# Optimization experiments

Hardware: AMD Instinct MI355X
Metric: run time of the kernel (lower is better)

## Reference

```python
import jax, jax.numpy as jnp
import numpy as np

D_MODEL = 1024
H = 16
D_H = D_MODEL // H


def setup_inputs() -> dict:
    key = jax.random.key(0)
    ks = jax.random.split(key, 10)
    B, T_dec, T_enc = 2, 2048, 2048
    s = 1.0 / np.sqrt(D_MODEL)
    return {
        "tgt": jax.random.normal(ks[0], (B, T_dec, D_MODEL), jnp.float32),
        "memory": jax.random.normal(ks[1], (B, T_enc, D_MODEL), jnp.float32),
        "W_q": jax.random.normal(ks[2], (D_MODEL, D_MODEL), jnp.float32) * s,
        "b_q": jnp.zeros((D_MODEL,), jnp.float32),
        "W_k": jax.random.normal(ks[3], (D_MODEL, D_MODEL), jnp.float32) * s,
        "b_k": jnp.zeros((D_MODEL,), jnp.float32),
        "W_v": jax.random.normal(ks[4], (D_MODEL, D_MODEL), jnp.float32) * s,
        "b_v": jnp.zeros((D_MODEL,), jnp.float32),
        "W_o": jax.random.normal(ks[5], (D_MODEL, D_MODEL), jnp.float32) * s,
        "b_o": jnp.zeros((D_MODEL,), jnp.float32),
    }


def reference(tgt, memory, W_q, b_q, W_k, b_k, W_v, b_v, W_o, b_o):
    B, T_dec, _ = tgt.shape
    T_enc = memory.shape[1]
    # Projections (nn.Linear: x @ W^T + b; here W stored as (in,out) so x @ W + b)
    Q = tgt @ W_q + b_q          # (B, T_dec, d_model)
    K = memory @ W_k + b_k       # (B, T_enc, d_model)
    V = memory @ W_v + b_v       # (B, T_enc, d_model)
    # split heads: (B, h, T, d_h)
    Q = Q.reshape(B, T_dec, H, D_H).transpose(0, 2, 1, 3)
    K = K.reshape(B, T_enc, H, D_H).transpose(0, 2, 1, 3)
    V = V.reshape(B, T_enc, H, D_H).transpose(0, 2, 1, 3)
    # scores (B, h, T_dec, T_enc)
    S = jnp.einsum("bhqd,bhkd->bhqk", Q, K) / jnp.sqrt(jnp.float32(D_H)).astype(Q.dtype)
    A = jax.nn.softmax(S, axis=-1)
    Y = jnp.einsum("bhqk,bhkd->bhqd", A, V)
    Y = Y.transpose(0, 2, 1, 3).reshape(B, T_dec, D_MODEL)
    return Y @ W_o + b_o
```

## Files before the change

kernel.cpp:

```cpp
#include <hip/hip_runtime.h>
#include <hip/hip_bf16.h>
#include <stdint.h>

typedef unsigned short u16;
typedef __attribute__((ext_vector_type(8))) short bf16x8;
typedef __attribute__((ext_vector_type(4))) short bf16x4;
typedef __attribute__((ext_vector_type(4))) float f32x4;

__device__ __forceinline__ float bf2f(u16 u) {
    union { unsigned int i; float f; } v; v.i = ((unsigned int)u) << 16; return v.f;
}
__device__ __forceinline__ u16 f2bf(float f) {
    union { float f; unsigned int i; } v; v.f = f;
    unsigned int x = v.i;
    return (u16)((x + 0x7fffu + ((x >> 16) & 1u)) >> 16);
}
__device__ __forceinline__ unsigned fbits(float f) {
    union { float f; unsigned int i; } v; v.f = f; return v.i;
}
__device__ __forceinline__ void async16(const void* g, void* lds) {
    __builtin_amdgcn_global_load_lds((const __attribute__((address_space(1))) void*)g,
                                     (__attribute__((address_space(3))) void*)lds,
                                     16, 0, 0);
}

#define QSCALE 0.18033688f

__global__ __launch_bounds__(256) void prep(
    const float* __restrict__ tgt, const float* __restrict__ mem,
    const float* __restrict__ Wq, const float* __restrict__ Wk,
    const float* __restrict__ Wv, const float* __restrict__ Wo,
    u16* __restrict__ Wt, u16* __restrict__ tgtb, u16* __restrict__ memb)
{
    __shared__ u16 tile[64][65];
    const int id = blockIdx.x;
    const int tid = threadIdx.x;
    if (id < 1024) {
        const int z = id >> 8;
        const float* in = (z == 0) ? Wq : (z == 1) ? Wk : (z == 2) ? Wv : Wo;
        u16* out = Wt + (size_t)z * 1048576;
        const int k0 = (id & 15) * 64, n0 = ((id >> 4) & 15) * 64;
        const int r = tid >> 2, c0 = (tid & 3) << 4;
#pragma unroll
        for (int i = 0; i < 4; ++i) {
            float4 v = *(const float4*)&in[(size_t)(k0 + r) * 1024 + n0 + c0 + i * 4];
            tile[c0 + i * 4 + 0][r] = f2bf(v.x);
            tile[c0 + i * 4 + 1][r] = f2bf(v.y);
            tile[c0 + i * 4 + 2][r] = f2bf(v.z);
            tile[c0 + i * 4 + 3][r] = f2bf(v.w);
        }
        __syncthreads();
#pragma unroll
        for (int i = 0; i < 2; ++i) {
            bf16x8 v;
#pragma unroll
            for (int j = 0; j < 8; ++j) v[j] = (short)tile[r][c0 + i * 8 + j];
            *(bf16x8*)&out[(size_t)(n0 + r) * 1024 + k0 + c0 + i * 8] = v;
        }
    } else {
        size_t i = ((size_t)(id - 1024) * 256 + tid) * 8;
        float4 a0 = *(const float4*)&tgt[i];
        float4 a1 = *(const float4*)&tgt[i + 4];
        float4 b0 = *(const float4*)&mem[i];
        float4 b1 = *(const float4*)&mem[i + 4];
        bf16x8 va, vb;
        va[0] = (short)f2bf(a0.x); va[1] = (short)f2bf(a0.y);
        va[2] = (short)f2bf(a0.z); va[3] = (short)f2bf(a0.w);
        va[4] = (short)f2bf(a1.x); va[5] = (short)f2bf(a1.y);
        va[6] = (short)f2bf(a1.z); va[7] = (short)f2bf(a1.w);
        vb[0] = (short)f2bf(b0.x); vb[1] = (short)f2bf(b0.y);
        vb[2] = (short)f2bf(b0.z); vb[3] = (short)f2bf(b0.w);
        vb[4] = (short)f2bf(b1.x); vb[5] = (short)f2bf(b1.y);
        vb[6] = (short)f2bf(b1.z); vb[7] = (short)f2bf(b1.w);
        *(bf16x8*)&tgtb[i] = va;
        *(bf16x8*)&memb[i] = vb;
    }
}

__global__ __launch_bounds__(256) void gemm_qkv(
    const u16* __restrict__ tgtb, const u16* __restrict__ memb,
    const u16* __restrict__ Wt,
    const float* __restrict__ bq, const float* __restrict__ bk, const float* __restrict__ bv,
    u16* __restrict__ Qb, u16* __restrict__ Kb, u16* __restrict__ Vtb)
{
    __shared__ __align__(16) u16 sA[128 * 32];
    __shared__ __align__(16) u16 sB[128 * 32];
    const int z = blockIdx.z;
    const u16* A = (z == 0) ? tgtb : memb;
    const u16* Bt = Wt + (size_t)z * 1048576;
    const float* bias = (z == 0) ? bq : (z == 1) ? bk : bv;

    const int tid = threadIdx.x;
    const int wave = tid >> 6, lane = tid & 63;
    const int quad = lane >> 4, l16 = lane & 15;
    const int m0 = blockIdx.x * 128, n0 = blockIdx.y * 128;
    const int wm = (wave & 1) * 64, wn = (wave >> 1) * 64;
    const int sw = (quad ^ ((l16 >> 1) & 3)) << 3;

    f32x4 acc[4][4] = {};

    for (int k0 = 0; k0 < 1024; k0 += 32) {
        __syncthreads();
#pragma unroll
        for (int r = 0; r < 2; ++r) {
            int c = tid + r * 256;
            int g = (c & 3) ^ ((c >> 3) & 3);
            const u16* gA = A + (size_t)(m0 + (c >> 2)) * 1024 + k0 + g * 8;
            async16(gA, (char*)sA + r * 4096 + wave * 1024);
            const u16* gB = Bt + (size_t)(n0 + (c >> 2)) * 1024 + k0 + g * 8;
            async16(gB, (char*)sB + r * 4096 + wave * 1024);
        }
        __syncthreads();
        bf16x8 af[4], bfr[4];
#pragma unroll
        for (int i = 0; i < 4; ++i) {
            af[i]  = *(const bf16x8*)&sA[(wm + i * 16 + l16) * 32 + sw];
            bfr[i] = *(const bf16x8*)&sB[(wn + i * 16 + l16) * 32 + sw];
        }
#pragma unroll
        for (int i = 0; i < 4; ++i)
#pragma unroll
            for (int j = 0; j < 4; ++j)
                acc[i][j] = __builtin_amdgcn_mfma_f32_16x16x32_bf16(af[i], bfr[j], acc[i][j], 0, 0, 0);
    }

    if (z == 2) {
#pragma unroll
        for (int j = 0; j < 4; ++j) {
            int n = n0 + wn + j * 16 + l16;
            float bb = bias[n];
            int d = n & 63;
#pragma unroll
            for (int i = 0; i < 4; ++i) {
                int mb = m0 + wm + i * 16 + quad * 4;
                int bh = (mb >> 11) * 16 + (n >> 6);
                bf16x4 pk;
#pragma unroll
                for (int r = 0; r < 4; ++r) pk[r] = (short)f2bf(acc[i][j][r] + bb);
                *(bf16x4*)&Vtb[(size_t)bh * 131072 + (size_t)d * 2048 + (mb & 2047)] = pk;
            }
        }
    } else {
        u16* C = (z == 0) ? Qb : Kb;
        const float scl = (z == 0) ? QSCALE : 1.0f;
#pragma unroll
        for (int j = 0; j < 4; ++j) {
            int n = n0 + wn + j * 16 + l16;
            float bb = bias[n];
#pragma unroll
            for (int i = 0; i < 4; ++i) {
                int mb = m0 + wm + i * 16 + quad * 4;
#pragma unroll
                for (int r = 0; r < 4; ++r)
                    C[(size_t)(mb + r) * 1024 + n] = f2bf((acc[i][j][r] + bb) * scl);
            }
        }
    }
}

__global__ __launch_bounds__(256) void gemm_out(
    const u16* __restrict__ A, const u16* __restrict__ Bt,
    const float* __restrict__ bias, float* __restrict__ C)
{
    __shared__ __align__(16) u16 sA[64 * 32];
    __shared__ __align__(16) u16 sB[128 * 32];
    const int tid = threadIdx.x;
    const int wave = tid >> 6, lane = tid & 63;
    const int quad = lane >> 4, l16 = lane & 15;
    const int m0 = blockIdx.x * 64, n0 = blockIdx.y * 128;
    const int wm = (wave & 1) * 32, wn = (wave >> 1) * 64;
    const int sw = (quad ^ ((l16 >> 1) & 3)) << 3;
    f32x4 acc[2][4] = {};

    for (int k0 = 0; k0 < 1024; k0 += 32) {
        __syncthreads();
        {
            int c = tid;
            int g = (c & 3) ^ ((c >> 3) & 3);
            const u16* gA = A + (size_t)(m0 + (c >> 2)) * 1024 + k0 + g * 8;
            async16(gA, (char*)sA + wave * 1024);
        }
#pragma unroll
        for (int r = 0; r < 2; ++r) {
            int c = tid + r * 256;
            int g = (c & 3) ^ ((c >> 3) & 3);
            const u16* gB = Bt + (size_t)(n0 + (c >> 2)) * 1024 + k0 + g * 8;
            async16(gB, (char*)sB + r * 4096 + wave * 1024);
        }
        __syncthreads();
        bf16x8 af[2], bfr[4];
#pragma unroll
        for (int i = 0; i < 2; ++i)
            af[i] = *(const bf16x8*)&sA[(wm + i * 16 + l16) * 32 + sw];
#pragma unroll
        for (int j = 0; j < 4; ++j)
            bfr[j] = *(const bf16x8*)&sB[(wn + j * 16 + l16) * 32 + sw];
#pragma unroll
        for (int i = 0; i < 2; ++i)
#pragma unroll
            for (int j = 0; j < 4; ++j)
                acc[i][j] = __builtin_amdgcn_mfma_f32_16x16x32_bf16(af[i], bfr[j], acc[i][j], 0, 0, 0);
    }
#pragma unroll
    for (int j = 0; j < 4; ++j) {
        int n = n0 + wn + j * 16 + l16;
        float bb = bias[n];
#pragma unroll
        for (int i = 0; i < 2; ++i) {
            int mb = m0 + wm + i * 16 + quad * 4;
#pragma unroll
            for (int r = 0; r < 4; ++r)
                C[(size_t)(mb + r) * 1024 + n] = acc[i][j][r] + bb;
        }
    }
}

__global__ __launch_bounds__(256, 2) void attn_kernel(
    const u16* __restrict__ Q,
    const u16* __restrict__ K,
    const u16* __restrict__ Vt,
    u16* __restrict__ Y)
{
    __shared__ __align__(16) u16 sK[2][4096];
    __shared__ __align__(16) u16 sV[2][4096];

    const int tid = threadIdx.x;
    const int wave = tid >> 6, lane = tid & 63;
    const int quad = lane >> 4, l16 = lane & 15;

    const int bidx = blockIdx.x;
    const int bh = (bidx & 7) * 4 + ((bidx >> 3) & 3);
    const int qt = bidx >> 5;
    const int b = bh >> 4, h = bh & 15;
    const size_t qrow0 = (size_t)b * 2048 + qt * 128;
    const int st = ((qt << 1) | (bh & 1)) & 31;

    const size_t qrowA = qrow0 + wave * 32 + l16;
    const size_t qrowB = qrowA + 16;
    bf16x8 qA0 = *(const bf16x8*)&Q[qrowA * 1024 + h * 64 + quad * 8];
    bf16x8 qA1 = *(const bf16x8*)&Q[qrowA * 1024 + h * 64 + 32 + quad * 8];
    bf16x8 qB0 = *(const bf16x8*)&Q[qrowB * 1024 + h * 64 + quad * 8];
    bf16x8 qB1 = *(const bf16x8*)&Q[qrowB * 1024 + h * 64 + 32 + quad * 8];

    f32x4 oA[4] = {}, oB[4] = {};
    float rowA = 0.0f, rowB = 0.0f;

    const u16* Kbase = K + (size_t)b * 2048 * 1024 + h * 64;
    const u16* Vbase = Vt + (size_t)bh * 131072;

    const int x7 = l16 & 7;
    int koff[2], voff[4];
#pragma unroll
    for (int kf = 0; kf < 2; ++kf)
        koff[kf] = (l16 * 8 + ((kf * 4 + quad) ^ x7)) * 8;
#pragma unroll
    for (int ks = 0; ks < 4; ++ks)
        voff[ks] = (l16 * 8 + ((ks * 2 + (quad >> 1)) ^ x7)) * 8 + (quad & 1) * 4;

#define STAGE1(kv0, buf, r)                                                   \
    {                                                                         \
        int c = tid + (r) * 256;                                              \
        int srow = c >> 3;                                                    \
        int g = (c & 7) ^ (srow & 7);                                         \
        async16(Kbase + (size_t)((kv0) + srow) * 1024 + g * 8,                \
                (char*)&sK[buf][0] + (r) * 4096 + wave * 1024);               \
        async16(Vbase + (size_t)srow * 2048 + (kv0) + g * 8,                  \
                (char*)&sV[buf][0] + (r) * 4096 + wave * 1024);               \
    }
#define STAGE(kv0, buf) STAGE1(kv0, buf, 0) STAGE1(kv0, buf, 1)

    STAGE(st * 64, 0);

    for (int i = 0; i < 32; ++i) {
        __syncthreads();
        if (i < 31) {
            int kvn = ((st + i + 1) & 31) * 64;
            STAGE(kvn, (i + 1) & 1);
        }
        const u16* kb = &sK[i & 1][0];
        const u16* vb = &sV[i & 1][0];

        bf16x8 kfr[4][2];
        bf16x4 vfr[4][4];
#pragma unroll
        for (int ks = 0; ks < 4; ++ks) {
            kfr[ks][0] = *(const bf16x8*)&kb[ks * 1024 + koff[0]];
            kfr[ks][1] = *(const bf16x8*)&kb[ks * 1024 + koff[1]];
        }
#pragma unroll
        for (int mt = 0; mt < 4; ++mt)
#pragma unroll
            for (int ks = 0; ks < 4; ++ks)
                vfr[mt][ks] = *(const bf16x4*)&vb[mt * 1024 + voff[ks]];

        __builtin_amdgcn_s_setprio(1);
#pragma unroll
        for (int ks = 0; ks < 4; ++ks) {
            f32x4 sA = {0.f, 0.f, 0.f, 0.f};
            f32x4 sB = {0.f, 0.f, 0.f, 0.f};
            sA = __builtin_amdgcn_mfma_f32_16x16x32_bf16(kfr[ks][0], qA0, sA, 0, 0, 0);
            sB = __builtin_amdgcn_mfma_f32_16x16x32_bf16(kfr[ks][0], qB0, sB, 0, 0, 0);
            sA = __builtin_amdgcn_mfma_f32_16x16x32_bf16(kfr[ks][1], qA1, sA, 0, 0, 0);
            sB = __builtin_amdgcn_mfma_f32_16x16x32_bf16(kfr[ks][1], qB1, sB, 0, 0, 0);
            float a0 = __builtin_amdgcn_exp2f(sA[0]);
            float a1 = __builtin_amdgcn_exp2f(sA[1]);
            float a2 = __builtin_amdgcn_exp2f(sA[2]);
            float a3 = __builtin_amdgcn_exp2f(sA[3]);
            float b0 = __builtin_amdgcn_exp2f(sB[0]);
            float b1 = __builtin_amdgcn_exp2f(sB[1]);
            float b2 = __builtin_amdgcn_exp2f(sB[2]);
            float b3 = __builtin_amdgcn_exp2f(sB[3]);
            rowA += (a0 + a1) + (a2 + a3);
            rowB += (b0 + b1) + (b2 + b3);
            unsigned loA = __builtin_amdgcn_perm(fbits(a1) + 0x8000u, fbits(a0) + 0x8000u, 0x07060302u);
            unsigned hiA = __builtin_amdgcn_perm(fbits(a3) + 0x8000u, fbits(a2) + 0x8000u, 0x07060302u);
            unsigned loB = __builtin_amdgcn_perm(fbits(b1) + 0x8000u, fbits(b0) + 0x8000u, 0x07060302u);
            unsigned hiB = __builtin_amdgcn_perm(fbits(b3) + 0x8000u, fbits(b2) + 0x8000u, 0x07060302u);
            union { unsigned u[2]; bf16x4 v; } pA, pB;
            pA.u[0] = loA; pA.u[1] = hiA;
            pB.u[0] = loB; pB.u[1] = hiB;
#pragma unroll
            for (int mt = 0; mt < 4; ++mt) {
                oA[mt] = __builtin_amdgcn_mfma_f32_16x16x16bf16_1k(vfr[mt][ks], pA.v, oA[mt], 0, 0, 0);
                oB[mt] = __builtin_amdgcn_mfma_f32_16x16x16bf16_1k(vfr[mt][ks], pB.v, oB[mt], 0, 0, 0);
            }
        }
        __builtin_amdgcn_s_setprio(0);
    }
#undef STAGE
#undef STAGE1

    rowA += __shfl_xor(rowA, 16, 64);
    rowA += __shfl_xor(rowA, 32, 64);
    rowB += __shfl_xor(rowB, 16, 64);
    rowB += __shfl_xor(rowB, 32, 64);
    const float invA = 1.0f / rowA;
    const float invB = 1.0f / rowB;

#pragma unroll
    for (int mt = 0; mt < 4; ++mt) {
        bf16x4 oa, ob;
#pragma unroll
        for (int r = 0; r < 4; ++r) {
            oa[r] = (short)f2bf(oA[mt][r] * invA);
            ob[r] = (short)f2bf(oB[mt][r] * invB);
        }
        *(bf16x4*)&Y[qrowA * 1024 + h * 64 + mt * 16 + quad * 4] = oa;
        *(bf16x4*)&Y[qrowB * 1024 + h * 64 + mt * 16 + quad * 4] = ob;
    }
}

extern "C" void kernel_launch(void* const* d_in, const int* in_sizes, int n_in,
                              void* d_out, int out_size, void* d_ws, size_t ws_size,
                              hipStream_t stream) {
    const float* tgt = (const float*)d_in[0];
    const float* mem = (const float*)d_in[1];
    const float* Wq  = (const float*)d_in[2];
    const float* bq  = (const float*)d_in[3];
    const float* Wk  = (const float*)d_in[4];
    const float* bk  = (const float*)d_in[5];
    const float* Wv  = (const float*)d_in[6];
    const float* bv  = (const float*)d_in[7];
    const float* Wo  = (const float*)d_in[8];
    const float* bo  = (const float*)d_in[9];

    u16* ws = (u16*)d_ws;
    const size_t SZ = 4194304;
    u16* Wt   = ws;
    u16* tgtb = ws + 4 * SZ;
    u16* memb = tgtb + SZ;
    u16* Qb   = memb + SZ;
    u16* Kb   = Qb + SZ;
    u16* Vtb  = Kb + SZ;
    u16* Yb   = Vtb + SZ;
    float* out = (float*)d_out;

    prep<<<dim3(3072), 256, 0, stream>>>(tgt, mem, Wq, Wk, Wv, Wo, Wt, tgtb, memb);
    gemm_qkv<<<dim3(32, 8, 3), 256, 0, stream>>>(tgtb, memb, Wt, bq, bk, bv, Qb, Kb, Vtb);
    attn_kernel<<<dim3(512), 256, 0, stream>>>(Qb, Kb, Vtb, Yb);
    gemm_out<<<dim3(64, 8), 256, 0, stream>>>(Yb, Wt + 3 * (size_t)1048576, bo, out);
}
```

Measured before the change: 218.2 us.

## Split attention KV range in two halves and merge partials in combine kernel

The attention kernel now processes only half of the 2048 keys per block and launches twice as many blocks (1024), writing unnormalized fp32 partial outputs and row sums to workspace. A new combine kernel adds the two partials, normalizes by the summed row sums and writes the bf16 Y for the output GEMM. The aim is more parallelism and occupancy for the attention stage. The cost is an extra launch and extra fp32 global traffic for the partial outputs, placed in workspace regions that reuse buffers no longer live.

```diff
diff --git a/kernel.cpp b/kernel.cpp
--- a/kernel.cpp
+++ b/kernel.cpp
@@ -219,7 +219,8 @@
     const u16* __restrict__ Q,
     const u16* __restrict__ K,
     const u16* __restrict__ Vt,
-    u16* __restrict__ Y)
+    float* __restrict__ O0, float* __restrict__ O1,
+    float* __restrict__ R0, float* __restrict__ R1)
 {
     __shared__ __align__(16) u16 sK[2][4096];
     __shared__ __align__(16) u16 sV[2][4096];
@@ -229,11 +230,14 @@
     const int quad = lane >> 4, l16 = lane & 15;
 
     const int bidx = blockIdx.x;
-    const int bh = (bidx & 7) * 4 + ((bidx >> 3) & 3);
-    const int qt = bidx >> 5;
+    const int half = bidx >> 9;
+    const int b9 = bidx & 511;
+    const int bh = (b9 & 7) * 4 + ((b9 >> 3) & 3);
+    const int qt = b9 >> 5;
     const int b = bh >> 4, h = bh & 15;
     const size_t qrow0 = (size_t)b * 2048 + qt * 128;
-    const int st = ((qt << 1) | (bh & 1)) & 31;
+    const int st = ((qt << 1) | (bh & 1)) & 15;
+    const int tbase = half * 16;
 
     const size_t qrowA = qrow0 + wave * 32 + l16;
     const size_t qrowB = qrowA + 16;
@@ -269,12 +273,12 @@
     }
 #define STAGE(kv0, buf) STAGE1(kv0, buf, 0) STAGE1(kv0, buf, 1)
 
-    STAGE(st * 64, 0);
-
-    for (int i = 0; i < 32; ++i) {
-        __syncthreads();
-        if (i < 31) {
-            int kvn = ((st + i + 1) & 31) * 64;
+    STAGE((tbase + st) * 64, 0);
+
+    for (int i = 0; i < 16; ++i) {
+        __syncthreads();
+        if (i < 15) {
+            int kvn = (tbase + ((st + i + 1) & 15)) * 64;
             STAGE(kvn, (i + 1) & 1);
         }
         const u16* kb = &sK[i & 1][0];
@@ -334,19 +338,43 @@
     rowA += __shfl_xor(rowA, 32, 64);
     rowB += __shfl_xor(rowB, 16, 64);
     rowB += __shfl_xor(rowB, 32, 64);
-    const float invA = 1.0f / rowA;
-    const float invB = 1.0f / rowB;
-
+
+    float* Op = half ? O1 : O0;
+    float* Rp = half ? R1 : R0;
+    const int qlocA = qt * 128 + wave * 32 + l16;
+    const size_t obaseA = ((size_t)bh * 2048 + qlocA) * 64;
+    const size_t obaseB = obaseA + 16 * 64;
 #pragma unroll
     for (int mt = 0; mt < 4; ++mt) {
-        bf16x4 oa, ob;
-#pragma unroll
-        for (int r = 0; r < 4; ++r) {
-            oa[r] = (short)f2bf(oA[mt][r] * invA);
-            ob[r] = (short)f2bf(oB[mt][r] * invB);
-        }
-        *(bf16x4*)&Y[qrowA * 1024 + h * 64 + mt * 16 + quad * 4] = oa;
-        *(bf16x4*)&Y[qrowB * 1024 + h * 64 + mt * 16 + quad * 4] = ob;
+        *(f32x4*)&Op[obaseA + mt * 16 + quad * 4] = oA[mt];
+        *(f32x4*)&Op[obaseB + mt * 16 + quad * 4] = oB[mt];
+    }
+    if (quad == 0) {
+        Rp[bh * 2048 + qlocA] = rowA;
+        Rp[bh * 2048 + qlocA + 16] = rowB;
+    }
+}
+
+__global__ __launch_bounds__(256) void combine(
+    const float* __restrict__ O0, const float* __restrict__ O1,
+    const float* __restrict__ R0, const float* __restrict__ R1,
+    u16* __restrict__ Y)
+{
+    const int t0 = blockIdx.x * 256 + threadIdx.x;
+#pragma unroll
+    for (int it = 0; it < 4; ++it) {
+        int g = t0 + it * 262144;
+        int m = g >> 4;
+        int dq = (g & 15) * 4;
+        int bh = m >> 11, qloc = m & 2047;
+        int b = bh >> 4, h = bh & 15;
+        f32x4 a = *(const f32x4*)&O0[(size_t)m * 64 + dq];
+        f32x4 c = *(const f32x4*)&O1[(size_t)m * 64 + dq];
+        float inv = 1.0f / (R0[m] + R1[m]);
+        bf16x4 y;
+#pragma unroll
+        for (int r = 0; r < 4; ++r) y[r] = (short)f2bf((a[r] + c[r]) * inv);
+        *(bf16x4*)&Y[((size_t)b * 2048 + qloc) * 1024 + h * 64 + dq] = y;
     }
 }
 
@@ -375,8 +403,14 @@
     u16* Yb   = Vtb + SZ;
     float* out = (float*)d_out;
 
+    float* O0 = (float*)(ws + SZ);
+    float* O1 = (float*)(ws + 3 * SZ);
+    float* R0 = (float*)(ws + 5 * SZ);
+    float* R1 = R0 + 65536;
+
     prep<<<dim3(3072), 256, 0, stream>>>(tgt, mem, Wq, Wk, Wv, Wo, Wt, tgtb, memb);
     gemm_qkv<<<dim3(32, 8, 3), 256, 0, stream>>>(tgtb, memb, Wt, bq, bk, bv, Qb, Kb, Vtb);
-    attn_kernel<<<dim3(512), 256, 0, stream>>>(Qb, Kb, Vtb, Yb);
+    attn_kernel<<<dim3(1024), 256, 0, stream>>>(Qb, Kb, Vtb, O0, O1, R0, R1);
+    combine<<<dim3(1024), 256, 0, stream>>>(O0, O1, R0, R1, Yb);
     gemm_out<<<dim3(64, 8), 256, 0, stream>>>(Yb, Wt + 3 * (size_t)1048576, bo, out);
 }
```

Measured after the change: 232.9 us. 1.07x slower.

## Double-buffer LDS tiles in QKV and output projection GEMMs

Applied to the files above, without the earlier changes.

Both projection GEMMs now keep two LDS buffers per operand. Each iteration issues the async global-to-LDS loads for the next K-slice before computing on the current one, which drops one of the two barriers per iteration. The aim is to overlap global memory latency with the MFMA work. In exchange, LDS use per block doubles, which may lower occupancy.

```diff
diff --git a/kernel.cpp b/kernel.cpp
--- a/kernel.cpp
+++ b/kernel.cpp
@@ -83,8 +83,8 @@
     const float* __restrict__ bq, const float* __restrict__ bk, const float* __restrict__ bv,
     u16* __restrict__ Qb, u16* __restrict__ Kb, u16* __restrict__ Vtb)
 {
-    __shared__ __align__(16) u16 sA[128 * 32];
-    __shared__ __align__(16) u16 sB[128 * 32];
+    __shared__ __align__(16) u16 sA[2][128 * 32];
+    __shared__ __align__(16) u16 sB[2][128 * 32];
     const int z = blockIdx.z;
     const u16* A = (z == 0) ? tgtb : memb;
     const u16* Bt = Wt + (size_t)z * 1048576;
@@ -99,23 +99,31 @@
 
     f32x4 acc[4][4] = {};
 
-    for (int k0 = 0; k0 < 1024; k0 += 32) {
+#define GSTAGE(k0, buf)                                                       \
+    {                                                                         \
+        _Pragma("unroll")                                                     \
+        for (int r = 0; r < 2; ++r) {                                         \
+            int c = tid + r * 256;                                            \
+            int g = (c & 3) ^ ((c >> 3) & 3);                                 \
+            const u16* gA = A + (size_t)(m0 + (c >> 2)) * 1024 + (k0) + g * 8;\
+            async16(gA, (char*)&sA[buf][0] + r * 4096 + wave * 1024);         \
+            const u16* gB = Bt + (size_t)(n0 + (c >> 2)) * 1024 + (k0) + g * 8;\
+            async16(gB, (char*)&sB[buf][0] + r * 4096 + wave * 1024);         \
+        }                                                                     \
+    }
+
+    GSTAGE(0, 0);
+
+    for (int it = 0; it < 32; ++it) {
         __syncthreads();
-#pragma unroll
-        for (int r = 0; r < 2; ++r) {
-            int c = tid + r * 256;
-            int g = (c & 3) ^ ((c >> 3) & 3);
-            const u16* gA = A + (size_t)(m0 + (c >> 2)) * 1024 + k0 + g * 8;
-            async16(gA, (char*)sA + r * 4096 + wave * 1024);
-            const u16* gB = Bt + (size_t)(n0 + (c >> 2)) * 1024 + k0 + g * 8;
-            async16(gB, (char*)sB + r * 4096 + wave * 1024);
-        }
-        __syncthreads();
+        if (it < 31) GSTAGE((it + 1) * 32, (it + 1) & 1);
+        const u16* a = &sA[it & 1][0];
+        const u16* bb_ = &sB[it & 1][0];
         bf16x8 af[4], bfr[4];
 #pragma unroll
         for (int i = 0; i < 4; ++i) {
-            af[i]  = *(const bf16x8*)&sA[(wm + i * 16 + l16) * 32 + sw];
-            bfr[i] = *(const bf16x8*)&sB[(wn + i * 16 + l16) * 32 + sw];
+            af[i]  = *(const bf16x8*)&a[(wm + i * 16 + l16) * 32 + sw];
+            bfr[i] = *(const bf16x8*)&bb_[(wn + i * 16 + l16) * 32 + sw];
         }
 #pragma unroll
         for (int i = 0; i < 4; ++i)
@@ -123,6 +131,7 @@
             for (int j = 0; j < 4; ++j)
                 acc[i][j] = __builtin_amdgcn_mfma_f32_16x16x32_bf16(af[i], bfr[j], acc[i][j], 0, 0, 0);
     }
+#undef GSTAGE
 
     if (z == 2) {
 #pragma unroll
@@ -162,8 +171,8 @@
     const u16* __restrict__ A, const u16* __restrict__ Bt,
     const float* __restrict__ bias, float* __restrict__ C)
 {
-    __shared__ __align__(16) u16 sA[64 * 32];
-    __shared__ __align__(16) u16 sB[128 * 32];
+    __shared__ __align__(16) u16 sA[2][64 * 32];
+    __shared__ __align__(16) u16 sB[2][128 * 32];
     const int tid = threadIdx.x;
     const int wave = tid >> 6, lane = tid & 63;
     const int quad = lane >> 4, l16 = lane & 15;
@@ -172,35 +181,45 @@
     const int sw = (quad ^ ((l16 >> 1) & 3)) << 3;
     f32x4 acc[2][4] = {};
 
-    for (int k0 = 0; k0 < 1024; k0 += 32) {
+#define OSTAGE(k0, buf)                                                       \
+    {                                                                         \
+        {                                                                     \
+            int c = tid;                                                      \
+            int g = (c & 3) ^ ((c >> 3) & 3);                                 \
+            const u16* gA = A + (size_t)(m0 + (c >> 2)) * 1024 + (k0) + g * 8;\
+            async16(gA, (char*)&sA[buf][0] + wave * 1024);                    \
+        }                                                                     \
+        _Pragma("unroll")                                                     \
+        for (int r = 0; r < 2; ++r) {                                         \
+            int c = tid + r * 256;                                            \
+            int g = (c & 3) ^ ((c >> 3) & 3);                                 \
+            const u16* gB = Bt + (size_t)(n0 + (c >> 2)) * 1024 + (k0) + g * 8;\
+            async16(gB, (char*)&sB[buf][0] + r * 4096 + wave * 1024);         \
+        }                                                                     \
+    }
+
+    OSTAGE(0, 0);
+
+    for (int it = 0; it < 32; ++it) {
         __syncthreads();
-        {
-            int c = tid;
-            int g = (c & 3) ^ ((c >> 3) & 3);
-            const u16* gA = A + (size_t)(m0 + (c >> 2)) * 1024 + k0 + g * 8;
-            async16(gA, (char*)sA + wave * 1024);
-        }
-#pragma unroll
-        for (int r = 0; r < 2; ++r) {
-            int c = tid + r * 256;
-            int g = (c & 3) ^ ((c >> 3) & 3);
-            const u16* gB = Bt + (size_t)(n0 + (c >> 2)) * 1024 + k0 + g * 8;
-            async16(gB, (char*)sB + r * 4096 + wave * 1024);
-        }
-        __syncthreads();
+        if (it < 31) OSTAGE((it + 1) * 32, (it + 1) & 1);
+        const u16* a = &sA[it & 1][0];
+        const u16* bb_ = &sB[it & 1][0];
         bf16x8 af[2], bfr[4];
 #pragma unroll
         for (int i = 0; i < 2; ++i)
-            af[i] = *(const bf16x8*)&sA[(wm + i * 16 + l16) * 32 + sw];
+            af[i] = *(const bf16x8*)&a[(wm + i * 16 + l16) * 32 + sw];
 #pragma unroll
         for (int j = 0; j < 4; ++j)
-            bfr[j] = *(const bf16x8*)&sB[(wn + j * 16 + l16) * 32 + sw];
+            bfr[j] = *(const bf16x8*)&bb_[(wn + j * 16 + l16) * 32 + sw];
 #pragma unroll
         for (int i = 0; i < 2; ++i)
 #pragma unroll
             for (int j = 0; j < 4; ++j)
                 acc[i][j] = __builtin_amdgcn_mfma_f32_16x16x32_bf16(af[i], bfr[j], acc[i][j], 0, 0, 0);
     }
+#undef OSTAGE
+
 #pragma unroll
     for (int j = 0; j < 4; ++j) {
         int n = n0 + wn + j * 16 + l16;
```

After: 220.3 us. Within noise of the previous version (+1.0%).
